# Performance work log

Measured on AMD Instinct MI355X. Metric: run time of the kernel, lower is better.

## Reference

```python
import jax, jax.numpy as jnp
import numpy as np

B, S, H, NH = 2, 2048, 1024, 16
HD = H // NH
ROTARY_DIM = 64
EPS = 1e-5
MINUS_INF = -10000.0


def _apply_rotary(q, k, rotary_dim):
    # q, k: [B, S, NH, HD]; GPT-NeoX style rotate_half on first rotary_dim dims
    pos = jnp.arange(S, dtype=jnp.float32)
    inv_freq = 1.0 / (10000.0 ** (jnp.arange(0, rotary_dim, 2, dtype=jnp.float32) / rotary_dim))
    freqs = pos[:, None] * inv_freq[None, :]                      # [S, rd/2]
    cos = jnp.concatenate([jnp.cos(freqs)] * 2, -1)[None, :, None, :]  # [1,S,1,rd]
    sin = jnp.concatenate([jnp.sin(freqs)] * 2, -1)[None, :, None, :]

    def rot(t):
        t_rot, t_pass = t[..., :rotary_dim], t[..., rotary_dim:]
        t1, t2 = jnp.split(t_rot, 2, axis=-1)
        rotated = jnp.concatenate([-t2, t1], axis=-1)
        return jnp.concatenate([t_rot * cos + rotated * sin, t_pass], axis=-1)

    return rot(q), rot(k)


def setup_inputs() -> dict:
    key = jax.random.key(0)
    ks = jax.random.split(key, 6)
    w_scale = 0.02
    return {
        "x": jax.random.normal(ks[0], (B, S, H), jnp.float32),
        "input_mask": jnp.ones((B, S), jnp.int32),
        "norm_w": jnp.ones((H,), jnp.float32),
        "norm_b": jnp.zeros((H,), jnp.float32),
        "attn_qkvw": jax.random.normal(ks[1], (H, 3 * H), jnp.float32) * w_scale,
        "attn_qkvb": jax.random.normal(ks[2], (3 * H,), jnp.float32) * w_scale,
        "attn_ow": jax.random.normal(ks[3], (H, H), jnp.float32) * w_scale,
        "attn_ob": jax.random.normal(ks[4], (H,), jnp.float32) * w_scale,
    }


def reference(x, input_mask, norm_w, norm_b, attn_qkvw, attn_qkvb, attn_ow, attn_ob):
    # pre-layernorm (qkv_gemm path with config.pre_layer_norm)
    mu = x.mean(-1, keepdims=True)
    var = x.var(-1, keepdims=True)
    xn = (x - mu) * jax.lax.rsqrt(var + EPS) * norm_w + norm_b

    # fused QKV projection
    qkv = xn @ attn_qkvw + attn_qkvb                       # [B,S,3H]
    q, k, v = jnp.split(qkv, 3, axis=-1)
    q = q.reshape(B, S, NH, HD)
    k = k.reshape(B, S, NH, HD)
    v = v.reshape(B, S, NH, HD)

    # rotary embedding on q,k
    q, k = _apply_rotary(q, k, ROTARY_DIM)

    # scaled scores + mask bias (1 - mask) * -10000 + triangular masking
    scale = 1.0 / np.sqrt(HD).astype(np.float32)
    scores = jnp.einsum("bqhd,bkhd->bhqk", q, k) * scale   # [B,NH,S,S]
    mask_bias = (1.0 - input_mask.astype(scores.dtype)) * MINUS_INF
    scores = scores + mask_bias[:, None, None, :]
    causal = jnp.tril(jnp.ones((S, S), bool))
    scores = jnp.where(causal[None, None], scores, MINUS_INF)

    probs = jax.nn.softmax(scores, axis=-1)
    ctx = jnp.einsum("bhqk,bkhd->bqhd", probs, v).reshape(B, S, H)

    # output projection (vector_matmul + bias)
    return ctx @ attn_ow + attn_ob
```

## Files before the change

### kernel.cpp

```cpp
#include <hip/hip_runtime.h>
#include <hip/hip_bf16.h>

#define B_  2
#define S_  2048
#define H_  1024
#define NH_ 16
#define HD_ 64
#define T_  (B_*S_)
#define H3_ (3*H_)

typedef float  floatx4 __attribute__((ext_vector_type(4)));
typedef __bf16 bf16x8  __attribute__((ext_vector_type(8)));

__device__ inline unsigned short f2bf_rn(float f) {
    union { float f; unsigned int u; } v; v.f = f;
    unsigned int u = v.u;
    u += 0x7fffu + ((u >> 16) & 1u);
    return (unsigned short)(u >> 16);
}
__device__ inline unsigned short f2bf_tr(float f) {
    union { float f; unsigned int u; } v; v.f = f;
    return (unsigned short)(v.u >> 16);
}
__device__ inline floatx4 fzero4() { floatx4 v; v[0]=0.f; v[1]=0.f; v[2]=0.f; v[3]=0.f; return v; }

__device__ inline void gload_lds16(const unsigned short* g, unsigned short* l) {
    __builtin_amdgcn_global_load_lds((const __attribute__((address_space(1))) unsigned int*)g,
                                     (__attribute__((address_space(3))) unsigned int*)l,
                                     16, 0, 0);
}

#define TLD 72
__global__ __launch_bounds__(256) void cvt_both_k(const float* __restrict__ qkvw,
                                                  const float* __restrict__ ow,
                                                  unsigned short* __restrict__ qkvwT,
                                                  unsigned short* __restrict__ owT) {
    __shared__ unsigned short Ts[64 * TLD];
    int id = blockIdx.x;
    const float* W; unsigned short* Wt; int N, nb, kb;
    if (id < 768) { W = qkvw; Wt = qkvwT; N = H3_; nb = (id % 48) * 64; kb = (id / 48) * 64; }
    else { id -= 768; W = ow; Wt = owT; N = H_; nb = (id % 16) * 64; kb = (id / 16) * 64; }
    const int K = H_;
    const int tid = threadIdx.x;
    #pragma unroll
    for (int p = 0; p < 4; p++) {
        const int krow = kb + p * 16 + (tid >> 4);
        const int ncol = (tid & 15) * 4;
        const float4 w = *reinterpret_cast<const float4*>(&W[(size_t)krow * N + nb + ncol]);
        Ts[(ncol + 0) * TLD + p * 16 + (tid >> 4)] = f2bf_rn(w.x);
        Ts[(ncol + 1) * TLD + p * 16 + (tid >> 4)] = f2bf_rn(w.y);
        Ts[(ncol + 2) * TLD + p * 16 + (tid >> 4)] = f2bf_rn(w.z);
        Ts[(ncol + 3) * TLD + p * 16 + (tid >> 4)] = f2bf_rn(w.w);
    }
    __syncthreads();
    #pragma unroll
    for (int p = 0; p < 2; p++) {
        const int n = (tid >> 3) + p * 32;
        const int k8 = (tid & 7) * 8;
        const uint4 v = *reinterpret_cast<const uint4*>(&Ts[n * TLD + k8]);
        *reinterpret_cast<uint4*>(&Wt[(size_t)(nb + n) * K + kb + k8]) = v;
    }
}

__global__ __launch_bounds__(256) void layernorm_k(const float* __restrict__ x,
                                                   const float* __restrict__ w,
                                                   const float* __restrict__ b,
                                                   unsigned short* __restrict__ xn) {
    const int t   = blockIdx.x;
    const int tid = threadIdx.x;
    const float4 v = reinterpret_cast<const float4*>(x + (size_t)t * H_)[tid];
    float s  = v.x + v.y + v.z + v.w;
    float s2 = v.x*v.x + v.y*v.y + v.z*v.z + v.w*v.w;
    for (int off = 32; off > 0; off >>= 1) {
        s  += __shfl_down(s,  off, 64);
        s2 += __shfl_down(s2, off, 64);
    }
    __shared__ float red[8];
    const int wave = tid >> 6, lane = tid & 63;
    if (lane == 0) { red[wave] = s; red[4 + wave] = s2; }
    __syncthreads();
    if (tid == 0) {
        red[0] = red[0] + red[1] + red[2] + red[3];
        red[4] = red[4] + red[5] + red[6] + red[7];
    }
    __syncthreads();
    const float mean = red[0] * (1.f / H_);
    const float var  = red[4] * (1.f / H_) - mean * mean;
    const float rstd = rsqrtf(var + 1e-5f);
    const float4 wv = reinterpret_cast<const float4*>(w)[tid];
    const float4 bv = reinterpret_cast<const float4*>(b)[tid];
    ushort4 o = make_ushort4(f2bf_rn((v.x - mean) * rstd * wv.x + bv.x),
                             f2bf_rn((v.y - mean) * rstd * wv.y + bv.y),
                             f2bf_rn((v.z - mean) * rstd * wv.z + bv.z),
                             f2bf_rn((v.w - mean) * rstd * wv.w + bv.w));
    reinterpret_cast<ushort4*>(xn + (size_t)t * H_)[tid] = o;
}

#define BM 128
#define BN 128

__device__ inline void gemm_core(const unsigned short* __restrict__ A,
                                 const unsigned short* __restrict__ Bt,
                                 int K, int mBase, int nBase,
                                 int tid, floatx4 acc[4][4],
                                 unsigned short* As0, unsigned short* As1,
                                 unsigned short* Bs0, unsigned short* Bs1) {
    const int lane = tid & 63;
    const int wave = tid >> 6;
    const int wr = wave >> 1, wc = wave & 1;
    const int srow = lane >> 2;
    const int scol = (lane & 3) * 8;
    const int mrow = lane & 15;
    const int koff = (lane >> 4) * 8;

    for (int kb = 0; kb < K; kb += 64) {
        __syncthreads();
        #pragma unroll
        for (int p = 0; p < 2; p++) {
            const int r = wave * 16 + p * 64;
            const size_t ga = (size_t)(mBase + r + srow) * K + kb + scol;
            const size_t gb = (size_t)(nBase + r + srow) * K + kb + scol;
            gload_lds16(&A [ga],      &As0[r * 32]);
            gload_lds16(&A [ga + 32], &As1[r * 32]);
            gload_lds16(&Bt[gb],      &Bs0[r * 32]);
            gload_lds16(&Bt[gb + 32], &Bs1[r * 32]);
        }
        __syncthreads();

        #pragma unroll
        for (int half = 0; half < 2; half++) {
            const unsigned short* As = half ? As1 : As0;
            const unsigned short* Bs = half ? Bs1 : Bs0;
            bf16x8 afrag[4], bfrag[4];
            #pragma unroll
            for (int mt = 0; mt < 4; mt++)
                afrag[mt] = *reinterpret_cast<const bf16x8*>(&As[(wr * 64 + mt * 16 + mrow) * 32 + koff]);
            #pragma unroll
            for (int nt = 0; nt < 4; nt++)
                bfrag[nt] = *reinterpret_cast<const bf16x8*>(&Bs[(wc * 64 + nt * 16 + mrow) * 32 + koff]);
            #pragma unroll
            for (int mt = 0; mt < 4; mt++)
                #pragma unroll
                for (int nt = 0; nt < 4; nt++)
                    acc[mt][nt] = __builtin_amdgcn_mfma_f32_16x16x32_bf16(afrag[mt], bfrag[nt], acc[mt][nt], 0, 0, 0);
        }
    }
}

__global__ __launch_bounds__(256) void gemm_qkv_k(const unsigned short* __restrict__ A,
                                                  const unsigned short* __restrict__ Bt,
                                                  const float* __restrict__ bias,
                                                  unsigned short* __restrict__ Qo,
                                                  unsigned short* __restrict__ Ko,
                                                  unsigned short* __restrict__ Vto) {
    __shared__ unsigned short As0[BM * 32], As1[BM * 32];
    __shared__ unsigned short Bs0[BN * 32], Bs1[BN * 32];

    const int tid  = threadIdx.x;
    const int lane = tid & 63;
    const int wave = tid >> 6;
    const int wr = wave >> 1, wc = wave & 1;
    const int mBase = blockIdx.y * BM;
    const int nBase = blockIdx.x * BN;

    floatx4 acc[4][4];
    #pragma unroll
    for (int i = 0; i < 4; i++)
        #pragma unroll
        for (int j = 0; j < 4; j++) acc[i][j] = fzero4();

    gemm_core(A, Bt, H_, mBase, nBase, tid, acc, As0, As1, Bs0, Bs1);

    const int col0 = lane & 15;
    const int r0   = (lane >> 4) * 4;
    const int hg   = (nBase + wc * 64) >> 6;
    const int sec  = hg >> 4;
    const int h    = hg & 15;

    float bs[4];
    #pragma unroll
    for (int nt = 0; nt < 4; nt++) bs[nt] = bias[nBase + wc * 64 + nt * 16 + col0];

    if (sec < 2) {
        unsigned short* dst = (sec == 0) ? Qo : Ko;
        const float if0 = __expf((float)col0        * (-0.2878231366f));
        const float if1 = __expf((float)(16 + col0) * (-0.2878231366f));
        #pragma unroll
        for (int mt = 0; mt < 4; mt++) {
            #pragma unroll
            for (int reg = 0; reg < 4; reg++) {
                const int t  = mBase + wr * 64 + mt * 16 + r0 + reg;
                const int bb = t >> 11;
                const int s  = t & (S_ - 1);
                float sn0, cs0, sn1, cs1;
                __sincosf((float)s * if0, &sn0, &cs0);
                __sincosf((float)s * if1, &sn1, &cs1);
                const float v0 = acc[mt][0][reg] + bs[0];
                const float v1 = acc[mt][1][reg] + bs[1];
                const float v2 = acc[mt][2][reg] + bs[2];
                const float v3 = acc[mt][3][reg] + bs[3];
                const float o0 = v0 * cs0 - v2 * sn0;
                const float o1 = v1 * cs1 - v3 * sn1;
                const float o2 = v2 * cs0 + v0 * sn0;
                const float o3 = v3 * cs1 + v1 * sn1;
                const size_t rb = ((size_t)(bb * NH_ + h) * S_ + s) * HD_;
                dst[rb +      col0] = f2bf_rn(o0);
                dst[rb + 16 + col0] = f2bf_rn(o1);
                dst[rb + 32 + col0] = f2bf_rn(o2);
                dst[rb + 48 + col0] = f2bf_rn(o3);
            }
        }
    } else {
        #pragma unroll
        for (int mt = 0; mt < 4; mt++) {
            const int t0 = mBase + wr * 64 + mt * 16 + r0;
            const int bb = t0 >> 11;
            const int s0 = t0 & (S_ - 1);
            #pragma unroll
            for (int nt = 0; nt < 4; nt++) {
                const int d = nt * 16 + col0;
                ushort4 o;
                o.x = f2bf_rn(acc[mt][nt][0] + bs[nt]);
                o.y = f2bf_rn(acc[mt][nt][1] + bs[nt]);
                o.z = f2bf_rn(acc[mt][nt][2] + bs[nt]);
                o.w = f2bf_rn(acc[mt][nt][3] + bs[nt]);
                *reinterpret_cast<ushort4*>(&Vto[((size_t)(bb * NH_ + h) * HD_ + d) * S_ + s0]) = o;
            }
        }
    }
}

__global__ __launch_bounds__(256) void gemm_proj_k(const unsigned short* __restrict__ A,
                                                   const unsigned short* __restrict__ Bt,
                                                   const float* __restrict__ bias,
                                                   float* __restrict__ Cf,
                                                   int M, int N, int K) {
    __shared__ unsigned short As0[BM * 32], As1[BM * 32];
    __shared__ unsigned short Bs0[BN * 32], Bs1[BN * 32];

    const int tid  = threadIdx.x;
    const int lane = tid & 63;
    const int wave = tid >> 6;
    const int wr = wave >> 1, wc = wave & 1;
    const int mBase = blockIdx.y * BM;
    const int nBase = blockIdx.x * BN;

    floatx4 acc[4][4];
    #pragma unroll
    for (int i = 0; i < 4; i++)
        #pragma unroll
        for (int j = 0; j < 4; j++) acc[i][j] = fzero4();

    gemm_core(A, Bt, K, mBase, nBase, tid, acc, As0, As1, Bs0, Bs1);

    const int col0 = lane & 15;
    const int r0   = (lane >> 4) * 4;
    #pragma unroll
    for (int mt = 0; mt < 4; mt++) {
        #pragma unroll
        for (int nt = 0; nt < 4; nt++) {
            const int gcol = nBase + wc * 64 + nt * 16 + col0;
            const float bsv = bias[gcol];
            #pragma unroll
            for (int reg = 0; reg < 4; reg++) {
                const int grow = mBase + wr * 64 + mt * 16 + r0 + reg;
                Cf[(size_t)grow * N + gcol] = acc[mt][nt][reg] + bsv;
            }
        }
    }
}

#define ALD 72
#define SCL2 0.1803368801f
#define MNEG -14427.0f

__global__ __launch_bounds__(256, 3) void attn_k(const unsigned short* __restrict__ Q,
                                                 const unsigned short* __restrict__ Kg,
                                                 const unsigned short* __restrict__ Vt,
                                                 const int* __restrict__ mask,
                                                 unsigned short* __restrict__ ctx) {
    const int id = blockIdx.x;
    const int bh = id & 31;
    const int v  = 31 - (id >> 5);
    const int b  = bh >> 4;
    const int h  = bh & 15;
    const int tid  = threadIdx.x;
    const int lane = tid & 63;
    const int wave = tid >> 6;

    __shared__ unsigned short Ks [2][64 * ALD];
    __shared__ unsigned short Vts[2][64 * ALD];
    __shared__ unsigned short Ps[4][16 * ALD];

    const size_t base = (size_t)bh * S_ * HD_;
    const int qbase = v * 64 + wave * 16;
    const int mrow = lane & 15;
    const int koff = (lane >> 4) * 8;
    const int r0   = (lane >> 4) * 4;
    const int col0 = lane & 15;

    bf16x8 qf0 = *reinterpret_cast<const bf16x8*>(&Q[base + (size_t)(qbase + mrow) * HD_ + koff]);
    bf16x8 qf1 = *reinterpret_cast<const bf16x8*>(&Q[base + (size_t)(qbase + mrow) * HD_ + 32 + koff]);

    bf16x8 onesf;
    {
        const __bf16 ov = (__bf16)((mrow == 0) ? 1.f : 0.f);
        #pragma unroll
        for (int q = 0; q < 8; q++) onesf[q] = ov;
    }

    floatx4 Oacc[4];
    floatx4 Lacc = fzero4();
    #pragma unroll
    for (int nt = 0; nt < 4; nt++) Oacc[nt] = fzero4();

    const int srow = tid >> 3;
    const int scol = (tid & 7) * 8;

    uint4 k00, k01, k10, k11, v00, v01, v10, v11;
    float mb00, mb01, mb02, mb03, mb10, mb11, mb12, mb13;
#define PF_TILE(TT, KR0, KR1, VR0, VR1, M0, M1, M2, M3) do {                                   \
        const int kb_ = (TT) * 64;                                                             \
        KR0 = *reinterpret_cast<const uint4*>(&Kg[base + (size_t)(kb_ + srow)      * HD_ + scol]); \
        KR1 = *reinterpret_cast<const uint4*>(&Kg[base + (size_t)(kb_ + srow + 32) * HD_ + scol]); \
        VR0 = *reinterpret_cast<const uint4*>(&Vt[base + (size_t)srow        * S_ + kb_ + scol]);  \
        VR1 = *reinterpret_cast<const uint4*>(&Vt[base + (size_t)(srow + 32) * S_ + kb_ + scol]);  \
        M0 = (1.f - (float)mask[b * S_ + kb_ +  0 + col0]) * MNEG;                             \
        M1 = (1.f - (float)mask[b * S_ + kb_ + 16 + col0]) * MNEG;                             \
        M2 = (1.f - (float)mask[b * S_ + kb_ + 32 + col0]) * MNEG;                             \
        M3 = (1.f - (float)mask[b * S_ + kb_ + 48 + col0]) * MNEG;                             \
    } while (0)
#define PREFETCH_MACRO(MI) do {                                                                \
        const int t0_ = min(2 * (MI), v);                                                      \
        const int t1_ = min(2 * (MI) + 1, v);                                                  \
        PF_TILE(t0_, k00, k01, v00, v01, mb00, mb01, mb02, mb03);                              \
        PF_TILE(t1_, k10, k11, v10, v11, mb10, mb11, mb12, mb13);                              \
    } while (0)

    const int nmac = (v + 2) >> 1;
    PREFETCH_MACRO(0);

    unsigned short* pw = Ps[wave];

    for (int mi = 0; mi < nmac; mi++) {
        if (mi) __syncthreads();
        *reinterpret_cast<uint4*>(&Ks [0][ srow       * ALD + scol]) = k00;
        *reinterpret_cast<uint4*>(&Ks [0][(srow + 32) * ALD + scol]) = k01;
        *reinterpret_cast<uint4*>(&Ks [1][ srow       * ALD + scol]) = k10;
        *reinterpret_cast<uint4*>(&Ks [1][(srow + 32) * ALD + scol]) = k11;
        *reinterpret_cast<uint4*>(&Vts[0][ srow       * ALD + scol]) = v00;
        *reinterpret_cast<uint4*>(&Vts[0][(srow + 32) * ALD + scol]) = v01;
        *reinterpret_cast<uint4*>(&Vts[1][ srow       * ALD + scol]) = v10;
        *reinterpret_cast<uint4*>(&Vts[1][(srow + 32) * ALD + scol]) = v11;
        __syncthreads();
        const float mc00 = mb00, mc01 = mb01, mc02 = mb02, mc03 = mb03;
        const float mc10 = mb10, mc11 = mb11, mc12 = mb12, mc13 = mb13;
        if (mi + 1 < nmac) PREFETCH_MACRO(mi + 1);

        #pragma unroll
        for (int half = 0; half < 2; half++) {
            const int kt = 2 * mi + half;
            if (half && kt > v) continue;
            const int kb = kt * 64;
            const unsigned short* ks = Ks [half];
            const unsigned short* vs = Vts[half];
            const float c0 = half ? mc10 : mc00;
            const float c1 = half ? mc11 : mc01;
            const float c2 = half ? mc12 : mc02;
            const float c3 = half ? mc13 : mc03;

            floatx4 sc[4];
            #pragma unroll
            for (int nt = 0; nt < 4; nt++) {
                const bf16x8 kf0 = *reinterpret_cast<const bf16x8*>(&ks[(nt * 16 + mrow) * ALD + koff]);
                const bf16x8 kf1 = *reinterpret_cast<const bf16x8*>(&ks[(nt * 16 + mrow) * ALD + 32 + koff]);
                floatx4 c = fzero4();
                c = __builtin_amdgcn_mfma_f32_16x16x32_bf16(qf0, kf0, c, 0, 0, 0);
                c = __builtin_amdgcn_mfma_f32_16x16x32_bf16(qf1, kf1, c, 0, 0, 0);
                sc[nt] = c;
            }
            #pragma unroll
            for (int nt = 0; nt < 4; nt++) {
                const float mbv = (nt == 0) ? c0 : (nt == 1) ? c1 : (nt == 2) ? c2 : c3;
                #pragma unroll
                for (int reg = 0; reg < 4; reg++)
                    sc[nt][reg] = sc[nt][reg] * SCL2 + mbv;
            }
            if (kt == v) {
                #pragma unroll
                for (int nt = 0; nt < 4; nt++) {
                    const int key = kb + nt * 16 + col0;
                    #pragma unroll
                    for (int reg = 0; reg < 4; reg++)
                        if (key > qbase + r0 + reg) sc[nt][reg] = MNEG;
                }
            }
            #pragma unroll
            for (int nt = 0; nt < 4; nt++)
                #pragma unroll
                for (int reg = 0; reg < 4; reg++)
                    pw[(r0 + reg) * ALD + nt * 16 + col0] = f2bf_tr(exp2f(sc[nt][reg]));
            const bf16x8 p0 = *reinterpret_cast<const bf16x8*>(&pw[mrow * ALD + koff]);
            const bf16x8 p1 = *reinterpret_cast<const bf16x8*>(&pw[mrow * ALD + 32 + koff]);
            #pragma unroll
            for (int nt = 0; nt < 4; nt++) {
                const bf16x8 vf0 = *reinterpret_cast<const bf16x8*>(&vs[(nt * 16 + mrow) * ALD + koff]);
                const bf16x8 vf1 = *reinterpret_cast<const bf16x8*>(&vs[(nt * 16 + mrow) * ALD + 32 + koff]);
                Oacc[nt] = __builtin_amdgcn_mfma_f32_16x16x32_bf16(p0, vf0, Oacc[nt], 0, 0, 0);
                Oacc[nt] = __builtin_amdgcn_mfma_f32_16x16x32_bf16(p1, vf1, Oacc[nt], 0, 0, 0);
            }
            Lacc = __builtin_amdgcn_mfma_f32_16x16x32_bf16(p0, onesf, Lacc, 0, 0, 0);
            Lacc = __builtin_amdgcn_mfma_f32_16x16x32_bf16(p1, onesf, Lacc, 0, 0, 0);
        }
    }
#undef PREFETCH_MACRO
#undef PF_TILE

    float rl[4];
    #pragma unroll
    for (int reg = 0; reg < 4; reg++) {
        const float lsum = __shfl(Lacc[reg], lane & 48, 64);
        rl[reg] = 1.f / lsum;
    }
    #pragma unroll
    for (int nt = 0; nt < 4; nt++)
        #pragma unroll
        for (int reg = 0; reg < 4; reg++) {
            const int q = qbase + r0 + reg;
            const int d = nt * 16 + col0;
            ctx[((size_t)b * S_ + q) * H_ + h * HD_ + d] = f2bf_rn(Oacc[nt][reg] * rl[reg]);
        }
}

extern "C" void kernel_launch(void* const* d_in, const int* in_sizes, int n_in,
                              void* d_out, int out_size, void* d_ws, size_t ws_size,
                              hipStream_t stream) {
    const float* x     = (const float*)d_in[0];
    const int*   mask  = (const int*)d_in[1];
    const float* normw = (const float*)d_in[2];
    const float* normb = (const float*)d_in[3];
    const float* qkvw  = (const float*)d_in[4];
    const float* qkvb  = (const float*)d_in[5];
    const float* ow    = (const float*)d_in[6];
    const float* ob    = (const float*)d_in[7];
    float* out = (float*)d_out;

    char* ws = (char*)d_ws;
    unsigned short* xn_bf   = (unsigned short*)(ws);
    unsigned short* qkvwT   = (unsigned short*)(ws + (8ull  << 20));
    unsigned short* owT     = (unsigned short*)(ws + (14ull << 20));
    unsigned short* Qb      = (unsigned short*)(ws + (16ull << 20));
    unsigned short* Kb      = (unsigned short*)(ws + (24ull << 20));
    unsigned short* Vtb     = (unsigned short*)(ws + (32ull << 20));
    unsigned short* ctx_bf  = (unsigned short*)(ws + (40ull << 20));

    cvt_both_k<<<1024, 256, 0, stream>>>(qkvw, ow, qkvwT, owT);
    layernorm_k<<<T_, 256, 0, stream>>>(x, normw, normb, xn_bf);
    gemm_qkv_k<<<dim3(H3_ / BN, T_ / BM), 256, 0, stream>>>(xn_bf, qkvwT, qkvb, Qb, Kb, Vtb);
    attn_k<<<1024, 256, 0, stream>>>(Qb, Kb, Vtb, mask, ctx_bf);
    gemm_proj_k<<<dim3(H_ / BN, T_ / BM), 256, 0, stream>>>(ctx_bf, owT, ob, out, T_, H_, H_);
}
```

Baseline: 199.1 us.

## Pair short causal query bands per attention block and fuse prep kernels

Attention blocks now process either one long query band or two complementary short bands, so each block does a more uniform amount of causal work and the grid shrinks from 1024 to 768 blocks. The layernorm and weight conversion/transposition kernels are merged into one launch with block-index dispatch. This targets load imbalance and tail effects in the causal attention plus one kernel-launch overhead. The paired blocks run their bands serially, adding an extra barrier and a longer per-block critical path.

Result: slower. 209.6 us (+5.3%).

```diff
diff --git a/kernel.cpp b/kernel.cpp
--- a/kernel.cpp
+++ b/kernel.cpp
@@ -31,69 +31,69 @@
 }
 
 #define TLD 72
-__global__ __launch_bounds__(256) void cvt_both_k(const float* __restrict__ qkvw,
-                                                  const float* __restrict__ ow,
-                                                  unsigned short* __restrict__ qkvwT,
-                                                  unsigned short* __restrict__ owT) {
-    __shared__ unsigned short Ts[64 * TLD];
-    int id = blockIdx.x;
-    const float* W; unsigned short* Wt; int N, nb, kb;
-    if (id < 768) { W = qkvw; Wt = qkvwT; N = H3_; nb = (id % 48) * 64; kb = (id / 48) * 64; }
-    else { id -= 768; W = ow; Wt = owT; N = H_; nb = (id % 16) * 64; kb = (id / 16) * 64; }
-    const int K = H_;
+__global__ __launch_bounds__(256) void prep_k(const float* __restrict__ x,
+                                              const float* __restrict__ nw,
+                                              const float* __restrict__ nb,
+                                              unsigned short* __restrict__ xn,
+                                              const float* __restrict__ qkvw,
+                                              const float* __restrict__ ow,
+                                              unsigned short* __restrict__ qkvwT,
+                                              unsigned short* __restrict__ owT) {
     const int tid = threadIdx.x;
-    #pragma unroll
-    for (int p = 0; p < 4; p++) {
-        const int krow = kb + p * 16 + (tid >> 4);
-        const int ncol = (tid & 15) * 4;
-        const float4 w = *reinterpret_cast<const float4*>(&W[(size_t)krow * N + nb + ncol]);
-        Ts[(ncol + 0) * TLD + p * 16 + (tid >> 4)] = f2bf_rn(w.x);
-        Ts[(ncol + 1) * TLD + p * 16 + (tid >> 4)] = f2bf_rn(w.y);
-        Ts[(ncol + 2) * TLD + p * 16 + (tid >> 4)] = f2bf_rn(w.z);
-        Ts[(ncol + 3) * TLD + p * 16 + (tid >> 4)] = f2bf_rn(w.w);
-    }
-    __syncthreads();
-    #pragma unroll
-    for (int p = 0; p < 2; p++) {
-        const int n = (tid >> 3) + p * 32;
-        const int k8 = (tid & 7) * 8;
-        const uint4 v = *reinterpret_cast<const uint4*>(&Ts[n * TLD + k8]);
-        *reinterpret_cast<uint4*>(&Wt[(size_t)(nb + n) * K + kb + k8]) = v;
-    }
-}
-
-__global__ __launch_bounds__(256) void layernorm_k(const float* __restrict__ x,
-                                                   const float* __restrict__ w,
-                                                   const float* __restrict__ b,
-                                                   unsigned short* __restrict__ xn) {
-    const int t   = blockIdx.x;
-    const int tid = threadIdx.x;
-    const float4 v = reinterpret_cast<const float4*>(x + (size_t)t * H_)[tid];
-    float s  = v.x + v.y + v.z + v.w;
-    float s2 = v.x*v.x + v.y*v.y + v.z*v.z + v.w*v.w;
-    for (int off = 32; off > 0; off >>= 1) {
-        s  += __shfl_down(s,  off, 64);
-        s2 += __shfl_down(s2, off, 64);
-    }
-    __shared__ float red[8];
-    const int wave = tid >> 6, lane = tid & 63;
-    if (lane == 0) { red[wave] = s; red[4 + wave] = s2; }
-    __syncthreads();
-    if (tid == 0) {
-        red[0] = red[0] + red[1] + red[2] + red[3];
-        red[4] = red[4] + red[5] + red[6] + red[7];
-    }
-    __syncthreads();
-    const float mean = red[0] * (1.f / H_);
-    const float var  = red[4] * (1.f / H_) - mean * mean;
-    const float rstd = rsqrtf(var + 1e-5f);
-    const float4 wv = reinterpret_cast<const float4*>(w)[tid];
-    const float4 bv = reinterpret_cast<const float4*>(b)[tid];
-    ushort4 o = make_ushort4(f2bf_rn((v.x - mean) * rstd * wv.x + bv.x),
-                             f2bf_rn((v.y - mean) * rstd * wv.y + bv.y),
-                             f2bf_rn((v.z - mean) * rstd * wv.z + bv.z),
-                             f2bf_rn((v.w - mean) * rstd * wv.w + bv.w));
-    reinterpret_cast<ushort4*>(xn + (size_t)t * H_)[tid] = o;
+    if (blockIdx.x < T_) {
+        const int t = blockIdx.x;
+        const float4 v = reinterpret_cast<const float4*>(x + (size_t)t * H_)[tid];
+        float s  = v.x + v.y + v.z + v.w;
+        float s2 = v.x*v.x + v.y*v.y + v.z*v.z + v.w*v.w;
+        for (int off = 32; off > 0; off >>= 1) {
+            s  += __shfl_down(s,  off, 64);
+            s2 += __shfl_down(s2, off, 64);
+        }
+        __shared__ float red[8];
+        const int wave = tid >> 6, lane = tid & 63;
+        if (lane == 0) { red[wave] = s; red[4 + wave] = s2; }
+        __syncthreads();
+        if (tid == 0) {
+            red[0] = red[0] + red[1] + red[2] + red[3];
+            red[4] = red[4] + red[5] + red[6] + red[7];
+        }
+        __syncthreads();
+        const float mean = red[0] * (1.f / H_);
+        const float var  = red[4] * (1.f / H_) - mean * mean;
+        const float rstd = rsqrtf(var + 1e-5f);
+        const float4 wv = reinterpret_cast<const float4*>(nw)[tid];
+        const float4 bv = reinterpret_cast<const float4*>(nb)[tid];
+        ushort4 o = make_ushort4(f2bf_rn((v.x - mean) * rstd * wv.x + bv.x),
+                                 f2bf_rn((v.y - mean) * rstd * wv.y + bv.y),
+                                 f2bf_rn((v.z - mean) * rstd * wv.z + bv.z),
+                                 f2bf_rn((v.w - mean) * rstd * wv.w + bv.w));
+        reinterpret_cast<ushort4*>(xn + (size_t)t * H_)[tid] = o;
+    } else {
+        __shared__ unsigned short Ts[64 * TLD];
+        int id = blockIdx.x - T_;
+        const float* W; unsigned short* Wt; int N, nbase, kb;
+        if (id < 768) { W = qkvw; Wt = qkvwT; N = H3_; nbase = (id % 48) * 64; kb = (id / 48) * 64; }
+        else { id -= 768; W = ow; Wt = owT; N = H_; nbase = (id % 16) * 64; kb = (id / 16) * 64; }
+        const int K = H_;
+        #pragma unroll
+        for (int p = 0; p < 4; p++) {
+            const int krow = kb + p * 16 + (tid >> 4);
+            const int ncol = (tid & 15) * 4;
+            const float4 w = *reinterpret_cast<const float4*>(&W[(size_t)krow * N + nbase + ncol]);
+            Ts[(ncol + 0) * TLD + p * 16 + (tid >> 4)] = f2bf_rn(w.x);
+            Ts[(ncol + 1) * TLD + p * 16 + (tid >> 4)] = f2bf_rn(w.y);
+            Ts[(ncol + 2) * TLD + p * 16 + (tid >> 4)] = f2bf_rn(w.z);
+            Ts[(ncol + 3) * TLD + p * 16 + (tid >> 4)] = f2bf_rn(w.w);
+        }
+        __syncthreads();
+        #pragma unroll
+        for (int p = 0; p < 2; p++) {
+            const int n = (tid >> 3) + p * 32;
+            const int k8 = (tid & 7) * 8;
+            const uint4 v = *reinterpret_cast<const uint4*>(&Ts[n * TLD + k8]);
+            *reinterpret_cast<uint4*>(&Wt[(size_t)(nbase + n) * K + kb + k8]) = v;
+        }
+    }
 }
 
 #define BM 128
@@ -279,28 +279,31 @@
                                                  const unsigned short* __restrict__ Vt,
                                                  const int* __restrict__ mask,
                                                  unsigned short* __restrict__ ctx) {
-    const int id = blockIdx.x;
-    const int bh = id & 31;
-    const int v  = 31 - (id >> 5);
-    const int b  = bh >> 4;
-    const int h  = bh & 15;
+    const int id   = blockIdx.x;
+    const int bh   = id & 31;
+    const int slot = id >> 5;
+    const int b    = bh >> 4;
+    const int h    = bh & 15;
     const int tid  = threadIdx.x;
     const int lane = tid & 63;
     const int wave = tid >> 6;
 
+    int v0, v1, nbands;
+    if (slot < 8)       { v0 = 31 - slot; v1 = 0;         nbands = 1; }
+    else if (slot < 16) { v0 = slot - 8;  v1 = 23 - slot; nbands = 2; }
+    else                { v0 = slot;      v1 = 0;         nbands = 1; }
+
     __shared__ unsigned short Ks [2][64 * ALD];
     __shared__ unsigned short Vts[2][64 * ALD];
     __shared__ unsigned short Ps[4][16 * ALD];
 
     const size_t base = (size_t)bh * S_ * HD_;
-    const int qbase = v * 64 + wave * 16;
     const int mrow = lane & 15;
     const int koff = (lane >> 4) * 8;
     const int r0   = (lane >> 4) * 4;
     const int col0 = lane & 15;
-
-    bf16x8 qf0 = *reinterpret_cast<const bf16x8*>(&Q[base + (size_t)(qbase + mrow) * HD_ + koff]);
-    bf16x8 qf1 = *reinterpret_cast<const bf16x8*>(&Q[base + (size_t)(qbase + mrow) * HD_ + 32 + koff]);
+    const int srow = tid >> 3;
+    const int scol = (tid & 7) * 8;
 
     bf16x8 onesf;
     {
@@ -309,16 +312,24 @@
         for (int q = 0; q < 8; q++) onesf[q] = ov;
     }
 
-    floatx4 Oacc[4];
-    floatx4 Lacc = fzero4();
-    #pragma unroll
-    for (int nt = 0; nt < 4; nt++) Oacc[nt] = fzero4();
-
-    const int srow = tid >> 3;
-    const int scol = (tid & 7) * 8;
-
-    uint4 k00, k01, k10, k11, v00, v01, v10, v11;
-    float mb00, mb01, mb02, mb03, mb10, mb11, mb12, mb13;
+    unsigned short* pw = Ps[wave];
+
+    for (int bi = 0; bi < 2; bi++) {
+        if (bi >= nbands) break;
+        const int v = bi ? v1 : v0;
+        const int qbase = v * 64 + wave * 16;
+        if (bi) __syncthreads();
+
+        bf16x8 qf0 = *reinterpret_cast<const bf16x8*>(&Q[base + (size_t)(qbase + mrow) * HD_ + koff]);
+        bf16x8 qf1 = *reinterpret_cast<const bf16x8*>(&Q[base + (size_t)(qbase + mrow) * HD_ + 32 + koff]);
+
+        floatx4 Oacc[4];
+        floatx4 Lacc = fzero4();
+        #pragma unroll
+        for (int nt = 0; nt < 4; nt++) Oacc[nt] = fzero4();
+
+        uint4 k00, k01, k10, k11, va00, va01, va10, va11;
+        float mb00, mb01, mb02, mb03, mb10, mb11, mb12, mb13;
 #define PF_TILE(TT, KR0, KR1, VR0, VR1, M0, M1, M2, M3) do {                                   \
         const int kb_ = (TT) * 64;                                                             \
         KR0 = *reinterpret_cast<const uint4*>(&Kg[base + (size_t)(kb_ + srow)      * HD_ + scol]); \
@@ -333,103 +344,102 @@
 #define PREFETCH_MACRO(MI) do {                                                                \
         const int t0_ = min(2 * (MI), v);                                                      \
         const int t1_ = min(2 * (MI) + 1, v);                                                  \
-        PF_TILE(t0_, k00, k01, v00, v01, mb00, mb01, mb02, mb03);                              \
-        PF_TILE(t1_, k10, k11, v10, v11, mb10, mb11, mb12, mb13);                              \
+        PF_TILE(t0_, k00, k01, va00, va01, mb00, mb01, mb02, mb03);                            \
+        PF_TILE(t1_, k10, k11, va10, va11, mb10, mb11, mb12, mb13);                            \
     } while (0)
 
-    const int nmac = (v + 2) >> 1;
-    PREFETCH_MACRO(0);
-
-    unsigned short* pw = Ps[wave];
-
-    for (int mi = 0; mi < nmac; mi++) {
-        if (mi) __syncthreads();
-        *reinterpret_cast<uint4*>(&Ks [0][ srow       * ALD + scol]) = k00;
-        *reinterpret_cast<uint4*>(&Ks [0][(srow + 32) * ALD + scol]) = k01;
-        *reinterpret_cast<uint4*>(&Ks [1][ srow       * ALD + scol]) = k10;
-        *reinterpret_cast<uint4*>(&Ks [1][(srow + 32) * ALD + scol]) = k11;
-        *reinterpret_cast<uint4*>(&Vts[0][ srow       * ALD + scol]) = v00;
-        *reinterpret_cast<uint4*>(&Vts[0][(srow + 32) * ALD + scol]) = v01;
-        *reinterpret_cast<uint4*>(&Vts[1][ srow       * ALD + scol]) = v10;
-        *reinterpret_cast<uint4*>(&Vts[1][(srow + 32) * ALD + scol]) = v11;
-        __syncthreads();
-        const float mc00 = mb00, mc01 = mb01, mc02 = mb02, mc03 = mb03;
-        const float mc10 = mb10, mc11 = mb11, mc12 = mb12, mc13 = mb13;
-        if (mi + 1 < nmac) PREFETCH_MACRO(mi + 1);
-
-        #pragma unroll
-        for (int half = 0; half < 2; half++) {
-            const int kt = 2 * mi + half;
-            if (half && kt > v) continue;
-            const int kb = kt * 64;
-            const unsigned short* ks = Ks [half];
-            const unsigned short* vs = Vts[half];
-            const float c0 = half ? mc10 : mc00;
-            const float c1 = half ? mc11 : mc01;
-            const float c2 = half ? mc12 : mc02;
-            const float c3 = half ? mc13 : mc03;
-
-            floatx4 sc[4];
-            #pragma unroll
-            for (int nt = 0; nt < 4; nt++) {
-                const bf16x8 kf0 = *reinterpret_cast<const bf16x8*>(&ks[(nt * 16 + mrow) * ALD + koff]);
-                const bf16x8 kf1 = *reinterpret_cast<const bf16x8*>(&ks[(nt * 16 + mrow) * ALD + 32 + koff]);
-                floatx4 c = fzero4();
-                c = __builtin_amdgcn_mfma_f32_16x16x32_bf16(qf0, kf0, c, 0, 0, 0);
-                c = __builtin_amdgcn_mfma_f32_16x16x32_bf16(qf1, kf1, c, 0, 0, 0);
-                sc[nt] = c;
-            }
-            #pragma unroll
-            for (int nt = 0; nt < 4; nt++) {
-                const float mbv = (nt == 0) ? c0 : (nt == 1) ? c1 : (nt == 2) ? c2 : c3;
-                #pragma unroll
-                for (int reg = 0; reg < 4; reg++)
-                    sc[nt][reg] = sc[nt][reg] * SCL2 + mbv;
-            }
-            if (kt == v) {
+        const int nmac = (v + 2) >> 1;
+        PREFETCH_MACRO(0);
+
+        for (int mi = 0; mi < nmac; mi++) {
+            if (mi) __syncthreads();
+            *reinterpret_cast<uint4*>(&Ks [0][ srow       * ALD + scol]) = k00;
+            *reinterpret_cast<uint4*>(&Ks [0][(srow + 32) * ALD + scol]) = k01;
+            *reinterpret_cast<uint4*>(&Ks [1][ srow       * ALD + scol]) = k10;
+            *reinterpret_cast<uint4*>(&Ks [1][(srow + 32) * ALD + scol]) = k11;
+            *reinterpret_cast<uint4*>(&Vts[0][ srow       * ALD + scol]) = va00;
+            *reinterpret_cast<uint4*>(&Vts[0][(srow + 32) * ALD + scol]) = va01;
+            *reinterpret_cast<uint4*>(&Vts[1][ srow       * ALD + scol]) = va10;
+            *reinterpret_cast<uint4*>(&Vts[1][(srow + 32) * ALD + scol]) = va11;
+            __syncthreads();
+            const float mc00 = mb00, mc01 = mb01, mc02 = mb02, mc03 = mb03;
+            const float mc10 = mb10, mc11 = mb11, mc12 = mb12, mc13 = mb13;
+            if (mi + 1 < nmac) PREFETCH_MACRO(mi + 1);
+
+            #pragma unroll
+            for (int half = 0; half < 2; half++) {
+                const int kt = 2 * mi + half;
+                if (half && kt > v) continue;
+                const int kb = kt * 64;
+                const unsigned short* ks = Ks [half];
+                const unsigned short* vs = Vts[half];
+                const float c0 = half ? mc10 : mc00;
+                const float c1 = half ? mc11 : mc01;
+                const float c2 = half ? mc12 : mc02;
+                const float c3 = half ? mc13 : mc03;
+
+                floatx4 sc[4];
                 #pragma unroll
                 for (int nt = 0; nt < 4; nt++) {
-                    const int key = kb + nt * 16 + col0;
+                    const bf16x8 kf0 = *reinterpret_cast<const bf16x8*>(&ks[(nt * 16 + mrow) * ALD + koff]);
+                    const bf16x8 kf1 = *reinterpret_cast<const bf16x8*>(&ks[(nt * 16 + mrow) * ALD + 32 + koff]);
+                    floatx4 c = fzero4();
+                    c = __builtin_amdgcn_mfma_f32_16x16x32_bf16(qf0, kf0, c, 0, 0, 0);
+                    c = __builtin_amdgcn_mfma_f32_16x16x32_bf16(qf1, kf1, c, 0, 0, 0);
+                    sc[nt] = c;
+                }
+                #pragma unroll
+                for (int nt = 0; nt < 4; nt++) {
+                    const float mbv = (nt == 0) ? c0 : (nt == 1) ? c1 : (nt == 2) ? c2 : c3;
                     #pragma unroll
                     for (int reg = 0; reg < 4; reg++)
-                        if (key > qbase + r0 + reg) sc[nt][reg] = MNEG;
+                        sc[nt][reg] = sc[nt][reg] * SCL2 + mbv;
                 }
+                if (kt == v) {
+                    #pragma unroll
+                    for (int nt = 0; nt < 4; nt++) {
+                        const int key = kb + nt * 16 + col0;
+                        #pragma unroll
+                        for (int reg = 0; reg < 4; reg++)
+                            if (key > qbase + r0 + reg) sc[nt][reg] = MNEG;
+                    }
+                }
+                #pragma unroll
+                for (int nt = 0; nt < 4; nt++)
+                    #pragma unroll
+                    for (int reg = 0; reg < 4; reg++)
+                        pw[(r0 + reg) * ALD + nt * 16 + col0] = f2bf_tr(exp2f(sc[nt][reg]));
+                const bf16x8 p0 = *reinterpret_cast<const bf16x8*>(&pw[mrow * ALD + koff]);
+                const bf16x8 p1 = *reinterpret_cast<const bf16x8*>(&pw[mrow * ALD + 32 + koff]);
+                #pragma unroll
+                for (int nt = 0; nt < 4; nt++) {
+                    const bf16x8 vf0 = *reinterpret_cast<const bf16x8*>(&vs[(nt * 16 + mrow) * ALD + koff]);
+                    const bf16x8 vf1 = *reinterpret_cast<const bf16x8*>(&vs[(nt * 16 + mrow) * ALD + 32 + koff]);
+                    Oacc[nt] = __builtin_amdgcn_mfma_f32_16x16x32_bf16(p0, vf0, Oacc[nt], 0, 0, 0);
+                    Oacc[nt] = __builtin_amdgcn_mfma_f32_16x16x32_bf16(p1, vf1, Oacc[nt], 0, 0, 0);
+                }
+                Lacc = __builtin_amdgcn_mfma_f32_16x16x32_bf16(p0, onesf, Lacc, 0, 0, 0);
+                Lacc = __builtin_amdgcn_mfma_f32_16x16x32_bf16(p1, onesf, Lacc, 0, 0, 0);
             }
-            #pragma unroll
-            for (int nt = 0; nt < 4; nt++)
-                #pragma unroll
-                for (int reg = 0; reg < 4; reg++)
-                    pw[(r0 + reg) * ALD + nt * 16 + col0] = f2bf_tr(exp2f(sc[nt][reg]));
-            const bf16x8 p0 = *reinterpret_cast<const bf16x8*>(&pw[mrow * ALD + koff]);
-            const bf16x8 p1 = *reinterpret_cast<const bf16x8*>(&pw[mrow * ALD + 32 + koff]);
-            #pragma unroll
-            for (int nt = 0; nt < 4; nt++) {
-                const bf16x8 vf0 = *reinterpret_cast<const bf16x8*>(&vs[(nt * 16 + mrow) * ALD + koff]);
-                const bf16x8 vf1 = *reinterpret_cast<const bf16x8*>(&vs[(nt * 16 + mrow) * ALD + 32 + koff]);
-                Oacc[nt] = __builtin_amdgcn_mfma_f32_16x16x32_bf16(p0, vf0, Oacc[nt], 0, 0, 0);
-                Oacc[nt] = __builtin_amdgcn_mfma_f32_16x16x32_bf16(p1, vf1, Oacc[nt], 0, 0, 0);
-            }
-            Lacc = __builtin_amdgcn_mfma_f32_16x16x32_bf16(p0, onesf, Lacc, 0, 0, 0);
-            Lacc = __builtin_amdgcn_mfma_f32_16x16x32_bf16(p1, onesf, Lacc, 0, 0, 0);
-        }
-    }
+        }
 #undef PREFETCH_MACRO
 #undef PF_TILE
 
-    float rl[4];
-    #pragma unroll
-    for (int reg = 0; reg < 4; reg++) {
-        const float lsum = __shfl(Lacc[reg], lane & 48, 64);
-        rl[reg] = 1.f / lsum;
-    }
-    #pragma unroll
-    for (int nt = 0; nt < 4; nt++)
+        float rl[4];
         #pragma unroll
         for (int reg = 0; reg < 4; reg++) {
-            const int q = qbase + r0 + reg;
-            const int d = nt * 16 + col0;
-            ctx[((size_t)b * S_ + q) * H_ + h * HD_ + d] = f2bf_rn(Oacc[nt][reg] * rl[reg]);
-        }
+            const float lsum = __shfl(Lacc[reg], lane & 48, 64);
+            rl[reg] = 1.f / lsum;
+        }
+        #pragma unroll
+        for (int nt = 0; nt < 4; nt++)
+            #pragma unroll
+            for (int reg = 0; reg < 4; reg++) {
+                const int q = qbase + r0 + reg;
+                const int d = nt * 16 + col0;
+                ctx[((size_t)b * S_ + q) * H_ + h * HD_ + d] = f2bf_rn(Oacc[nt][reg] * rl[reg]);
+            }
+    }
 }
 
 extern "C" void kernel_launch(void* const* d_in, const int* in_sizes, int n_in,
@@ -454,9 +464,8 @@
     unsigned short* Vtb     = (unsigned short*)(ws + (32ull << 20));
     unsigned short* ctx_bf  = (unsigned short*)(ws + (40ull << 20));
 
-    cvt_both_k<<<1024, 256, 0, stream>>>(qkvw, ow, qkvwT, owT);
-    layernorm_k<<<T_, 256, 0, stream>>>(x, normw, normb, xn_bf);
+    prep_k<<<T_ + 1024, 256, 0, stream>>>(x, normw, normb, xn_bf, qkvw, ow, qkvwT, owT);
     gemm_qkv_k<<<dim3(H3_ / BN, T_ / BM), 256, 0, stream>>>(xn_bf, qkvwT, qkvb, Qb, Kb, Vtb);
-    attn_k<<<1024, 256, 0, stream>>>(Qb, Kb, Vtb, mask, ctx_bf);
+    attn_k<<<768, 256, 0, stream>>>(Qb, Kb, Vtb, mask, ctx_bf);
     gemm_proj_k<<<dim3(H_ / BN, T_ / BM), 256, 0, stream>>>(ctx_bf, owT, ob, out, T_, H_, H_);
 }
```
